# Performance work log

Hardware: AMD Instinct MI355X
Metric: run time of the kernel (lower is better)

## Reference

```python
import jax, jax.numpy as jnp
import numpy as np

N_NODES = 100000
N_EDGES = 1600000
IN_FEATS = 256
HEADS = 4
OUT_FEATS = 32


def setup_inputs() -> dict:
    key = jax.random.key(0)
    k1, k2, k3, k4, k5, k6 = jax.random.split(key, 6)
    feat = jax.random.normal(k1, (N_NODES, IN_FEATS), dtype=jnp.float32)
    fc_w = jax.random.normal(k2, (HEADS * OUT_FEATS, IN_FEATS), dtype=jnp.float32) * (1.0 / np.sqrt(IN_FEATS))
    attn_l = jax.random.normal(k3, (1, HEADS, OUT_FEATS), dtype=jnp.float32) * 0.1
    attn_r = jax.random.normal(k4, (1, HEADS, OUT_FEATS), dtype=jnp.float32) * 0.1
    src = jax.random.randint(k5, (N_EDGES,), 0, N_NODES, dtype=jnp.int32)
    dst = jax.random.randint(k6, (N_EDGES,), 0, N_NODES, dtype=jnp.int32)
    return {"feat": feat, "fc_w": fc_w, "attn_l": attn_l, "attn_r": attn_r, "src": src, "dst": dst}


def reference(feat, fc_w, attn_l, attn_r, src, dst):
    # feat: [N, F_in]; fc_w: [H*D, F_in]; attn_l/r: [1, H, D]; src/dst: [E]
    N = feat.shape[0]
    H, D = attn_l.shape[1], attn_l.shape[2]
    # linear projection (no bias), viewed as [N, H, D]
    ft = (feat @ fc_w.T).reshape(N, H, D)
    # per-node attention logits
    el = jnp.einsum('nhd,hd->nh', ft, attn_l[0])  # [N, H]
    er = jnp.einsum('nhd,hd->nh', ft, attn_r[0])  # [N, H]
    # per-edge score: leaky_relu(el[src] + er[dst])
    e = jax.nn.leaky_relu(el[src] + er[dst], negative_slope=0.2)  # [E, H]
    # edge softmax over incoming edges of each dst node (stable)
    emax = jax.ops.segment_max(e, dst, num_segments=N)  # [N, H]
    a = jnp.exp(e - emax[dst])  # [E, H]
    asum = jax.ops.segment_sum(a, dst, num_segments=N)  # [N, H]
    a = a / asum[dst]
    # attn_drop is a no-op in eval mode; weighted scatter-sum aggregation
    msg = ft[src] * a[:, :, None]  # [E, H, D]
    out = jax.ops.segment_sum(msg, dst, num_segments=N)  # [N, H, D]
    # final_layer=False, activation=None, norm=None -> flatten heads
    return out.reshape(N, H * D)
```

## Files before the change

### kernel.cpp

```cpp
#include <hip/hip_runtime.h>
#include <hip/hip_bf16.h>
#include <float.h>

#define IN_F 256
#define HD   128
#define NH   4

typedef __bf16 bf16x8 __attribute__((ext_vector_type(8)));
typedef __bf16 bf16x2 __attribute__((ext_vector_type(2)));
typedef float  f32x4  __attribute__((ext_vector_type(4)));

__global__ __launch_bounds__(256) void gemm_ft_mfma(const float* __restrict__ feat,
                                                    const float* __restrict__ w,
                                                    __bf16* __restrict__ ft, int N) {
    __shared__ __align__(16) __bf16 Bs[128][264];
    __shared__ __align__(16) __bf16 As[64][40];
    const int t = threadIdx.x;
    const int wv = t >> 6;
    const int lane = t & 63;
    const int row0 = blockIdx.x * 64;

    {
        const int col = t >> 1;
        const int koff = (t & 1) * 128;
        const float* wp = w + (size_t)col * IN_F + koff;
#pragma unroll
        for (int i = 0; i < 128; i += 8) {
            const float4 v0 = *(const float4*)(wp + i);
            const float4 v1 = *(const float4*)(wp + i + 4);
            bf16x8 b;
            b[0] = (__bf16)v0.x; b[1] = (__bf16)v0.y; b[2] = (__bf16)v0.z; b[3] = (__bf16)v0.w;
            b[4] = (__bf16)v1.x; b[5] = (__bf16)v1.y; b[6] = (__bf16)v1.z; b[7] = (__bf16)v1.w;
            *(bf16x8*)&Bs[col][koff + i] = b;
        }
    }

    f32x4 acc[8];
#pragma unroll
    for (int i = 0; i < 8; ++i) acc[i] = {0.f, 0.f, 0.f, 0.f};

    const int ar = t >> 2;
    const int ac = (t & 3) * 8;
    const int frow = (lane & 15);
    const int fk   = (lane >> 4) * 8;

    for (int ks = 0; ks < 8; ++ks) {
        const int k0 = ks * 32;
        __syncthreads();
        bf16x8 av;
        if (row0 + ar < N) {
            const float* fp = feat + (size_t)(row0 + ar) * IN_F + k0 + ac;
            const float4 v0 = *(const float4*)(fp);
            const float4 v1 = *(const float4*)(fp + 4);
            av[0] = (__bf16)v0.x; av[1] = (__bf16)v0.y; av[2] = (__bf16)v0.z; av[3] = (__bf16)v0.w;
            av[4] = (__bf16)v1.x; av[5] = (__bf16)v1.y; av[6] = (__bf16)v1.z; av[7] = (__bf16)v1.w;
        } else {
#pragma unroll
            for (int i = 0; i < 8; ++i) av[i] = (__bf16)0.f;
        }
        *(bf16x8*)&As[ar][ac] = av;
        __syncthreads();

        const bf16x8 af = *(const bf16x8*)&As[wv * 16 + frow][fk];
#pragma unroll
        for (int ct = 0; ct < 8; ++ct) {
            const bf16x8 bfrag = *(const bf16x8*)&Bs[ct * 16 + frow][k0 + fk];
            acc[ct] = __builtin_amdgcn_mfma_f32_16x16x32_bf16(af, bfrag, acc[ct], 0, 0, 0);
        }
    }

    const int mbase = row0 + wv * 16 + (lane >> 4) * 4;
    const int cbase = lane & 15;
#pragma unroll
    for (int ct = 0; ct < 8; ++ct) {
#pragma unroll
        for (int reg = 0; reg < 4; ++reg) {
            const int m = mbase + reg;
            if (m < N) ft[(size_t)m * HD + ct * 16 + cbase] = (__bf16)acc[ct][reg];
        }
    }
}

__global__ __launch_bounds__(256) void eler_k(const __bf16* __restrict__ ft,
                                              const float* __restrict__ attn_l,
                                              const float* __restrict__ attn_r,
                                              float* __restrict__ el,
                                              float* __restrict__ er, int N) {
    const int lane = threadIdx.x & 63;
    const int node = blockIdx.x * 4 + (threadIdx.x >> 6);
    if (node >= N) return;
    const bf16x2 f  = *(const bf16x2*)(ft + (size_t)node * HD + lane * 2);
    const float2 al = *(const float2*)(attn_l + lane * 2);
    const float2 ar = *(const float2*)(attn_r + lane * 2);
    const float fx = (float)f[0], fy = (float)f[1];
    float pl = fx * al.x + fy * al.y;
    float pr = fx * ar.x + fy * ar.y;
#pragma unroll
    for (int s = 1; s < 16; s <<= 1) {
        pl += __shfl_xor(pl, s);
        pr += __shfl_xor(pr, s);
    }
    if ((lane & 15) == 0) {
        const int h = lane >> 4;
        el[(size_t)node * NH + h] = pl;
        er[(size_t)node * NH + h] = pr;
    }
}

__global__ __launch_bounds__(256) void deg_rank_k(const int* __restrict__ dst,
                                                  int* __restrict__ deg,
                                                  int* __restrict__ rank, int E) {
    const int i = blockIdx.x * 256 + threadIdx.x;
    if (i < E) rank[i] = atomicAdd(&deg[dst[i]], 1);
}

__global__ __launch_bounds__(1024) void scan1_k(const int* __restrict__ deg,
                                                int* __restrict__ off,
                                                int* __restrict__ bsum, int N) {
    __shared__ int lds[1024];
    const int t = threadIdx.x;
    const int g = blockIdx.x * 1024 + t;
    const int x = (g < N) ? deg[g] : 0;
    lds[t] = x;
    __syncthreads();
    int v = x;
    for (int s = 1; s < 1024; s <<= 1) {
        const int add = (t >= s) ? lds[t - s] : 0;
        __syncthreads();
        v += add;
        lds[t] = v;
        __syncthreads();
    }
    if (g < N) off[g] = v - x;
    if (t == 1023) bsum[blockIdx.x] = v;
}

__global__ __launch_bounds__(128) void scan2_k(const int* __restrict__ bsum,
                                               int* __restrict__ boff, int nb) {
    __shared__ int lds[128];
    const int t = threadIdx.x;
    const int x = (t < nb) ? bsum[t] : 0;
    lds[t] = x;
    __syncthreads();
    int v = x;
    for (int s = 1; s < 128; s <<= 1) {
        const int add = (t >= s) ? lds[t - s] : 0;
        __syncthreads();
        v += add;
        lds[t] = v;
        __syncthreads();
    }
    boff[t] = v - x;
}

__global__ __launch_bounds__(256) void scatter_k(const int* __restrict__ src,
                                                 const int* __restrict__ dst,
                                                 const int* __restrict__ off,
                                                 const int* __restrict__ boff,
                                                 const int* __restrict__ rank,
                                                 int* __restrict__ ssrc, int E) {
    const int i = blockIdx.x * 256 + threadIdx.x;
    if (i < E) {
        const int d = dst[i];
        const int p = off[d] + boff[d >> 10] + rank[i];
        ssrc[p] = src[i];
    }
}

__global__ __launch_bounds__(64) void aggregate_k(const __bf16* __restrict__ ft,
                                                  const float* __restrict__ el,
                                                  const float* __restrict__ er,
                                                  const int* __restrict__ deg,
                                                  const int* __restrict__ off,
                                                  const int* __restrict__ boff,
                                                  const int* __restrict__ ssrc,
                                                  float* __restrict__ out, int N) {
    const int n = blockIdx.x;
    const int lane = threadIdx.x;
    float2* outp = (float2*)(out + (size_t)n * HD);
    const int dn = deg[n];
    if (dn == 0) {
        outp[lane] = make_float2(0.f, 0.f);
        return;
    }
    const int start = off[n] + boff[n >> 10];
    const float4 er4 = *(const float4*)(er + (size_t)n * NH);

    __shared__ float a_lds[64 * NH];
    __shared__ int   s_lds[64];
    float4 ssum = make_float4(0.f, 0.f, 0.f, 0.f);
    float2 acc = make_float2(0.f, 0.f);
    const int h = lane >> 4;

    for (int c0 = 0; c0 < dn; c0 += 64) {
        const int j = c0 + lane;
        if (j < dn) {
            const int sv = ssrc[start + j];
            s_lds[lane] = sv;
            float4 e = *(const float4*)(el + (size_t)sv * NH);
            e.x += er4.x; e.y += er4.y; e.z += er4.z; e.w += er4.w;
            e.x = e.x >= 0.f ? e.x : 0.2f * e.x;
            e.y = e.y >= 0.f ? e.y : 0.2f * e.y;
            e.z = e.z >= 0.f ? e.z : 0.2f * e.z;
            e.w = e.w >= 0.f ? e.w : 0.2f * e.w;
            float4 a;
            a.x = __expf(e.x); a.y = __expf(e.y);
            a.z = __expf(e.z); a.w = __expf(e.w);
            ssum.x += a.x; ssum.y += a.y; ssum.z += a.z; ssum.w += a.w;
            *(float4*)(a_lds + lane * NH) = a;
        }
        __syncthreads();
        const int cnt = min(64, dn - c0);
        for (int j2 = 0; j2 < cnt; ++j2) {
            const int sv = s_lds[j2];
            const float aj = a_lds[j2 * NH + h];
            const bf16x2 f = *(const bf16x2*)(ft + (size_t)sv * HD + lane * 2);
            acc.x = fmaf(aj, (float)f[0], acc.x);
            acc.y = fmaf(aj, (float)f[1], acc.y);
        }
        __syncthreads();
    }
#pragma unroll
    for (int s = 1; s < 64; s <<= 1) {
        ssum.x += __shfl_xor(ssum.x, s);
        ssum.y += __shfl_xor(ssum.y, s);
        ssum.z += __shfl_xor(ssum.z, s);
        ssum.w += __shfl_xor(ssum.w, s);
    }
    const float sumh = (h == 0) ? ssum.x : (h == 1) ? ssum.y : (h == 2) ? ssum.z : ssum.w;
    const float inv = 1.f / sumh;
    outp[lane] = make_float2(acc.x * inv, acc.y * inv);
}

extern "C" void kernel_launch(void* const* d_in, const int* in_sizes, int n_in,
                              void* d_out, int out_size, void* d_ws, size_t ws_size,
                              hipStream_t stream) {
    const float* feat   = (const float*)d_in[0];
    const float* fc_w   = (const float*)d_in[1];
    const float* attn_l = (const float*)d_in[2];
    const float* attn_r = (const float*)d_in[3];
    const int*   src    = (const int*)d_in[4];
    const int*   dst    = (const int*)d_in[5];
    const int N = in_sizes[0] / IN_F;
    const int E = in_sizes[4];
    float* out = (float*)d_out;

    char* wp = (char*)d_ws;
    __bf16* ft = (__bf16*)wp; wp += (size_t)N * HD * 2;
    float* el  = (float*)wp; wp += (size_t)N * NH * 4;
    float* er  = (float*)wp; wp += (size_t)N * NH * 4;
    int* deg   = (int*)wp;   wp += (size_t)N * 4;
    int* off   = (int*)wp;   wp += (size_t)N * 4;
    int* bsum  = (int*)wp;   wp += 1024;
    int* boff  = (int*)wp;   wp += 1024;
    int* rank  = (int*)wp;   wp += (size_t)E * 4;
    int* ssrc  = (int*)wp;   wp += (size_t)E * 4;

    hipMemsetAsync(deg, 0, (size_t)N * 4, stream);

    gemm_ft_mfma<<<dim3((N + 63) / 64), dim3(256), 0, stream>>>(feat, fc_w, ft, N);
    eler_k<<<dim3((N + 3) / 4), dim3(256), 0, stream>>>(ft, attn_l, attn_r, el, er, N);
    deg_rank_k<<<dim3((E + 255) / 256), dim3(256), 0, stream>>>(dst, deg, rank, E);
    const int nblk = (N + 1023) >> 10;
    scan1_k<<<dim3(nblk), dim3(1024), 0, stream>>>(deg, off, bsum, N);
    scan2_k<<<dim3(1), dim3(128), 0, stream>>>(bsum, boff, nblk);
    scatter_k<<<dim3((E + 255) / 256), dim3(256), 0, stream>>>(src, dst, off, boff, rank, ssrc, E);
    aggregate_k<<<dim3(N), dim3(64), 0, stream>>>(ft, el, er, deg, off, boff, ssrc, out, N);
}
```

Measured before the change: 402.5 us.

## Make GEMM persistent with 128-row tiles and vectorize edge aggregation gathers

```diff
diff --git a/kernel.cpp b/kernel.cpp
--- a/kernel.cpp
+++ b/kernel.cpp
@@ -5,20 +5,28 @@
 #define IN_F 256
 #define HD   128
 #define NH   4
+#define GM   128
 
 typedef __bf16 bf16x8 __attribute__((ext_vector_type(8)));
 typedef __bf16 bf16x2 __attribute__((ext_vector_type(2)));
 typedef float  f32x4  __attribute__((ext_vector_type(4)));
 
+__device__ __forceinline__ bf16x8 cvt8(const float4 a, const float4 b) {
+    bf16x8 r;
+    r[0] = (__bf16)a.x; r[1] = (__bf16)a.y; r[2] = (__bf16)a.z; r[3] = (__bf16)a.w;
+    r[4] = (__bf16)b.x; r[5] = (__bf16)b.y; r[6] = (__bf16)b.z; r[7] = (__bf16)b.w;
+    return r;
+}
+
 __global__ __launch_bounds__(256) void gemm_ft_mfma(const float* __restrict__ feat,
                                                     const float* __restrict__ w,
-                                                    __bf16* __restrict__ ft, int N) {
+                                                    __bf16* __restrict__ ft,
+                                                    int N, int ntiles) {
     __shared__ __align__(16) __bf16 Bs[128][264];
-    __shared__ __align__(16) __bf16 As[64][40];
+    __shared__ __align__(16) __bf16 As[GM][40];
     const int t = threadIdx.x;
     const int wv = t >> 6;
     const int lane = t & 63;
-    const int row0 = blockIdx.x * 64;
 
     {
         const int col = t >> 1;
@@ -28,56 +36,63 @@
         for (int i = 0; i < 128; i += 8) {
             const float4 v0 = *(const float4*)(wp + i);
             const float4 v1 = *(const float4*)(wp + i + 4);
-            bf16x8 b;
-            b[0] = (__bf16)v0.x; b[1] = (__bf16)v0.y; b[2] = (__bf16)v0.z; b[3] = (__bf16)v0.w;
-            b[4] = (__bf16)v1.x; b[5] = (__bf16)v1.y; b[6] = (__bf16)v1.z; b[7] = (__bf16)v1.w;
-            *(bf16x8*)&Bs[col][koff + i] = b;
+            *(bf16x8*)&Bs[col][koff + i] = cvt8(v0, v1);
         }
     }
 
-    f32x4 acc[8];
-#pragma unroll
-    for (int i = 0; i < 8; ++i) acc[i] = {0.f, 0.f, 0.f, 0.f};
-
-    const int ar = t >> 2;
-    const int ac = (t & 3) * 8;
-    const int frow = (lane & 15);
+    const int ar = t >> 1;
+    const int ac = (t & 1) * 16;
+    const int frow = lane & 15;
     const int fk   = (lane >> 4) * 8;
 
-    for (int ks = 0; ks < 8; ++ks) {
-        const int k0 = ks * 32;
-        __syncthreads();
-        bf16x8 av;
-        if (row0 + ar < N) {
-            const float* fp = feat + (size_t)(row0 + ar) * IN_F + k0 + ac;
-            const float4 v0 = *(const float4*)(fp);
-            const float4 v1 = *(const float4*)(fp + 4);
-            av[0] = (__bf16)v0.x; av[1] = (__bf16)v0.y; av[2] = (__bf16)v0.z; av[3] = (__bf16)v0.w;
-            av[4] = (__bf16)v1.x; av[5] = (__bf16)v1.y; av[6] = (__bf16)v1.z; av[7] = (__bf16)v1.w;
-        } else {
-#pragma unroll
-            for (int i = 0; i < 8; ++i) av[i] = (__bf16)0.f;
+    for (int tile = blockIdx.x; tile < ntiles; tile += gridDim.x) {
+        const int row0 = tile * GM;
+        f32x4 acc[2][8];
+#pragma unroll
+        for (int mt = 0; mt < 2; ++mt)
+#pragma unroll
+            for (int ct = 0; ct < 8; ++ct) acc[mt][ct] = {0.f, 0.f, 0.f, 0.f};
+
+        for (int ks = 0; ks < 8; ++ks) {
+            const int k0 = ks * 32;
+            __syncthreads();
+            bf16x8 av0, av1;
+            const int gr = row0 + ar;
+            if (gr < N) {
+                const float* fp = feat + (size_t)gr * IN_F + k0 + ac;
+                const float4 v0 = *(const float4*)(fp);
+                const float4 v1 = *(const float4*)(fp + 4);
+                const float4 v2 = *(const float4*)(fp + 8);
+                const float4 v3 = *(const float4*)(fp + 12);
+                av0 = cvt8(v0, v1);
+                av1 = cvt8(v2, v3);
+            } else {
+#pragma unroll
+                for (int i = 0; i < 8; ++i) { av0[i] = (__bf16)0.f; av1[i] = (__bf16)0.f; }
+            }
+            *(bf16x8*)&As[ar][ac] = av0;
+            *(bf16x8*)&As[ar][ac + 8] = av1;
+            __syncthreads();
+
+            const bf16x8 af0 = *(const bf16x8*)&As[wv * 32 + frow][fk];
+            const bf16x8 af1 = *(const bf16x8*)&As[wv * 32 + 16 + frow][fk];
+#pragma unroll
+            for (int ct = 0; ct < 8; ++ct) {
+                const bf16x8 bfrag = *(const bf16x8*)&Bs[ct * 16 + frow][k0 + fk];
+                acc[0][ct] = __builtin_amdgcn_mfma_f32_16x16x32_bf16(af0, bfrag, acc[0][ct], 0, 0, 0);
+                acc[1][ct] = __builtin_amdgcn_mfma_f32_16x16x32_bf16(af1, bfrag, acc[1][ct], 0, 0, 0);
+            }
         }
-        *(bf16x8*)&As[ar][ac] = av;
-        __syncthreads();
-
-        const bf16x8 af = *(const bf16x8*)&As[wv * 16 + frow][fk];
-#pragma unroll
-        for (int ct = 0; ct < 8; ++ct) {
-            const bf16x8 bfrag = *(const bf16x8*)&Bs[ct * 16 + frow][k0 + fk];
-            acc[ct] = __builtin_amdgcn_mfma_f32_16x16x32_bf16(af, bfrag, acc[ct], 0, 0, 0);
-        }
-    }
-
-    const int mbase = row0 + wv * 16 + (lane >> 4) * 4;
-    const int cbase = lane & 15;
-#pragma unroll
-    for (int ct = 0; ct < 8; ++ct) {
-#pragma unroll
-        for (int reg = 0; reg < 4; ++reg) {
-            const int m = mbase + reg;
-            if (m < N) ft[(size_t)m * HD + ct * 16 + cbase] = (__bf16)acc[ct][reg];
-        }
+        const int rb = row0 + wv * 32 + (lane >> 4) * 4;
+#pragma unroll
+        for (int mt = 0; mt < 2; ++mt)
+#pragma unroll
+            for (int ct = 0; ct < 8; ++ct)
+#pragma unroll
+                for (int reg = 0; reg < 4; ++reg) {
+                    const int m = rb + mt * 16 + reg;
+                    if (m < N) ft[(size_t)m * HD + ct * 16 + frow] = (__bf16)acc[mt][ct][reg];
+                }
     }
 }
 
@@ -177,10 +192,13 @@
                                                   float* __restrict__ out, int N) {
     const int n = blockIdx.x;
     const int lane = threadIdx.x;
-    float2* outp = (float2*)(out + (size_t)n * HD);
+    const int il = lane & 15;
+    const int q  = lane >> 4;
+    const int h  = il >> 2;
+    float4* outp = (float4*)(out + (size_t)n * HD);
     const int dn = deg[n];
     if (dn == 0) {
-        outp[lane] = make_float2(0.f, 0.f);
+        if (q < 2) outp[il * 2 + q] = make_float4(0.f, 0.f, 0.f, 0.f);
         return;
     }
     const int start = off[n] + boff[n >> 10];
@@ -189,34 +207,43 @@
     __shared__ float a_lds[64 * NH];
     __shared__ int   s_lds[64];
     float4 ssum = make_float4(0.f, 0.f, 0.f, 0.f);
-    float2 acc = make_float2(0.f, 0.f);
-    const int h = lane >> 4;
+    float acc[8];
+#pragma unroll
+    for (int i = 0; i < 8; ++i) acc[i] = 0.f;
 
     for (int c0 = 0; c0 < dn; c0 += 64) {
         const int j = c0 + lane;
+        float4 a = make_float4(0.f, 0.f, 0.f, 0.f);
+        int sv = 0;
         if (j < dn) {
-            const int sv = ssrc[start + j];
-            s_lds[lane] = sv;
+            sv = ssrc[start + j];
             float4 e = *(const float4*)(el + (size_t)sv * NH);
             e.x += er4.x; e.y += er4.y; e.z += er4.z; e.w += er4.w;
             e.x = e.x >= 0.f ? e.x : 0.2f * e.x;
             e.y = e.y >= 0.f ? e.y : 0.2f * e.y;
             e.z = e.z >= 0.f ? e.z : 0.2f * e.z;
             e.w = e.w >= 0.f ? e.w : 0.2f * e.w;
-            float4 a;
             a.x = __expf(e.x); a.y = __expf(e.y);
             a.z = __expf(e.z); a.w = __expf(e.w);
             ssum.x += a.x; ssum.y += a.y; ssum.z += a.z; ssum.w += a.w;
-            *(float4*)(a_lds + lane * NH) = a;
         }
+        s_lds[lane] = sv;
+        *(float4*)(a_lds + lane * NH) = a;
         __syncthreads();
         const int cnt = min(64, dn - c0);
-        for (int j2 = 0; j2 < cnt; ++j2) {
-            const int sv = s_lds[j2];
-            const float aj = a_lds[j2 * NH + h];
-            const bf16x2 f = *(const bf16x2*)(ft + (size_t)sv * HD + lane * 2);
-            acc.x = fmaf(aj, (float)f[0], acc.x);
-            acc.y = fmaf(aj, (float)f[1], acc.y);
+        for (int j2 = 0; j2 < cnt; j2 += 8) {
+            const int e0 = j2 + q;
+            const int e1 = j2 + 4 + q;
+            const int sv0 = s_lds[e0];
+            const int sv1 = s_lds[e1];
+            const float a0 = a_lds[e0 * NH + h];
+            const float a1 = a_lds[e1 * NH + h];
+            const bf16x8 f0 = *(const bf16x8*)(ft + (size_t)sv0 * HD + il * 8);
+            const bf16x8 f1 = *(const bf16x8*)(ft + (size_t)sv1 * HD + il * 8);
+#pragma unroll
+            for (int k = 0; k < 8; ++k) acc[k] = fmaf(a0, (float)f0[k], acc[k]);
+#pragma unroll
+            for (int k = 0; k < 8; ++k) acc[k] = fmaf(a1, (float)f1[k], acc[k]);
         }
         __syncthreads();
     }
@@ -227,9 +254,18 @@
         ssum.z += __shfl_xor(ssum.z, s);
         ssum.w += __shfl_xor(ssum.w, s);
     }
+#pragma unroll
+    for (int k = 0; k < 8; ++k) {
+        acc[k] += __shfl_xor(acc[k], 16);
+        acc[k] += __shfl_xor(acc[k], 32);
+    }
     const float sumh = (h == 0) ? ssum.x : (h == 1) ? ssum.y : (h == 2) ? ssum.z : ssum.w;
     const float inv = 1.f / sumh;
-    outp[lane] = make_float2(acc.x * inv, acc.y * inv);
+    if (q < 2) {
+        const int b = q * 4;
+        outp[il * 2 + q] = make_float4(acc[b] * inv, acc[b + 1] * inv,
+                                       acc[b + 2] * inv, acc[b + 3] * inv);
+    }
 }
 
 extern "C" void kernel_launch(void* const* d_in, const int* in_sizes, int n_in,
@@ -258,7 +294,8 @@
 
     hipMemsetAsync(deg, 0, (size_t)N * 4, stream);
 
-    gemm_ft_mfma<<<dim3((N + 63) / 64), dim3(256), 0, stream>>>(feat, fc_w, ft, N);
+    const int ntiles = (N + GM - 1) / GM;
+    gemm_ft_mfma<<<dim3(512), dim3(256), 0, stream>>>(feat, fc_w, ft, N, ntiles);
     eler_k<<<dim3((N + 3) / 4), dim3(256), 0, stream>>>(ft, attn_l, attn_r, el, er, N);
     deg_rank_k<<<dim3((E + 255) / 256), dim3(256), 0, stream>>>(dst, deg, rank, E);
     const int nblk = (N + 1023) >> 10;
```

Result: faster. 385.9 us (-4.1%).
